# Kernel tuning notes

Hardware: AMD Instinct MI355X
Metric: run time of the kernel (lower is better)

## Reference

```python
import jax, jax.numpy as jnp
import numpy as np

# Dimensions: T total prefill tokens, S ragged segments (one adapter each),
# M target modules sharing this linear, r LoRA rank.
T, D_IN, D_OUT, R, M, S = 8192, 4096, 4096, 16, 2, 8


def setup_inputs() -> dict:
    key = jax.random.key(0)
    ks = jax.random.split(key, 6)
    x = jax.random.normal(ks[0], (T, D_IN), dtype=jnp.float32)
    W = jax.random.normal(ks[1], (D_OUT, D_IN), dtype=jnp.float32) * 0.02
    b = jax.random.normal(ks[2], (D_OUT,), dtype=jnp.float32) * 0.02
    # lora_A[m, s] = A.T of adapter s for target module m: [D_IN, R]
    lora_A = jax.random.normal(ks[3], (M, S, D_IN, R), dtype=jnp.float32) * 0.02
    # lora_B[m, s] = B.T: [R, D_OUT]
    lora_B = jax.random.normal(ks[4], (M, S, R, D_OUT), dtype=jnp.float32) * 0.02
    cu = jnp.sort(jax.random.randint(ks[5], (S + 1,), 0, T + 1, dtype=jnp.int32))
    cu = cu.at[0].set(0).at[-1].set(T)  # segment boundaries cover [0, T)
    return {"x": x, "W": W, "b": b, "lora_A": lora_A, "lora_B": lora_B,
            "cu_seqlen": cu}


def reference(x, W, b, lora_A, lora_B, cu_seqlen):
    # Base linear: out = x @ W.T + b
    out = x @ W.T + b
    tok = jnp.arange(x.shape[0])
    n_seg = lora_A.shape[1]
    # SGMV-style ragged LoRA: tokens in segment s use adapter s for every
    # target module m; contributions from all modules add into `out`.
    # Masking (instead of dynamic slicing) keeps shapes static / jit-friendly
    # and is exact: masked-out tokens contribute zero.
    for s in range(n_seg):
        mask = ((tok >= cu_seqlen[s]) & (tok < cu_seqlen[s + 1]))
        xm = x * mask.astype(x.dtype)[:, None]            # [T, D_IN], zero outside segment
        u = jnp.einsum('td,mdr->tmr', xm, lora_A[:, s])    # [T, M, R] low-rank down-proj
        out = out + jnp.einsum('tmr,mrD->tD', u, lora_B[:, s])  # up-proj, sum over modules
    return out
```

## Files before the change

kernel.cpp:

```cpp
#include <hip/hip_runtime.h>
#include <hip/hip_bf16.h>

#define T_TOK 8192
#define DIN   4096
#define DOUT  4096
#define RANK  16
#define NMOD  2
#define NSEG  8

typedef __attribute__((ext_vector_type(8))) short bf16x8;
typedef __attribute__((ext_vector_type(8))) unsigned short u16x8;
typedef __attribute__((ext_vector_type(4))) float f32x4;

__device__ inline unsigned short f2bf(float f) {
    union { float f; unsigned u; } v; v.f = f;
    unsigned r = v.u + 0x7FFFu + ((v.u >> 16) & 1u);
    return (unsigned short)(r >> 16);
}

__device__ inline void gload_lds16(const void* g, void* l) {
    __builtin_amdgcn_global_load_lds(
        (const __attribute__((address_space(1))) void*)g,
        (__attribute__((address_space(3))) void*)l, 16, 0, 0);
}

__global__ void cast2_bf16_kernel(const float* __restrict__ sa,
                                  unsigned short* __restrict__ da, int n8a,
                                  const float* __restrict__ sb,
                                  unsigned short* __restrict__ db, int n8b) {
    int i = blockIdx.x * blockDim.x + threadIdx.x;
    const float* s;
    unsigned short* d;
    size_t j;
    if (i < n8a) { s = sa; d = da; j = (size_t)i; }
    else if (i < n8a + n8b) { s = sb; d = db; j = (size_t)(i - n8a); }
    else return;
    const float4* s4 = (const float4*)s;
    float4 a = s4[2 * j];
    float4 b = s4[2 * j + 1];
    u16x8 o;
    o[0] = f2bf(a.x); o[1] = f2bf(a.y); o[2] = f2bf(a.z); o[3] = f2bf(a.w);
    o[4] = f2bf(b.x); o[5] = f2bf(b.y); o[6] = f2bf(b.z); o[7] = f2bf(b.w);
    *(u16x8*)(d + 8 * j) = o;
}

__global__ void prep_A_kernel(const float* __restrict__ A,
                              unsigned short* __restrict__ At) {
    int idx = blockIdx.x * 256 + threadIdx.x;
    int d   = idx & (DIN - 1);
    int smr = idx >> 12;
    int s   = smr >> 5, mr = smr & 31;
    int m   = mr >> 4,  r  = mr & 15;
    float v = A[(((size_t)(m * NSEG + s) * DIN) + d) * RANK + r];
    At[idx] = f2bf(v);
}

__global__ void prep_B_kernel(const float* __restrict__ B,
                              unsigned short* __restrict__ Bt) {
    int o  = blockIdx.x * 256 + threadIdx.x;
    int s  = o >> 12;
    int oc = o & (DOUT - 1);
    unsigned short tmp[32];
    for (int m = 0; m < NMOD; ++m)
        for (int r = 0; r < RANK; ++r)
            tmp[m * 16 + r] =
                f2bf(B[(((size_t)(m * NSEG + s) * RANK) + r) * DOUT + oc]);
    for (int k = 0; k < 4; ++k) {
        u16x8 v;
        for (int j = 0; j < 8; ++j) v[j] = tmp[k * 8 + j];
        *(u16x8*)(Bt + (size_t)o * 32 + k * 8) = v;
    }
}

__global__ __launch_bounds__(64) void u_gemm_kernel(
    const unsigned short* __restrict__ xb, const unsigned short* __restrict__ At,
    const int* __restrict__ cu, float* __restrict__ Pu) {
    int tile = blockIdx.x;
    int ky   = blockIdx.y;
    int lane = threadIdx.x;
    int l15  = lane & 15, lk = lane >> 4;
    int t0   = tile * 32;
    f32x4 acc[2][2] = {};
    bf16x8 zero = {};
    for (int s = 0; s < NSEG; ++s) {
        int lo = cu[s], hi = cu[s + 1];
        if (hi <= t0 || lo >= t0 + 32) continue;
        const unsigned short* atb = At + (size_t)(s * 32) * DIN;
        for (int kt = 0; kt < 32; ++kt) {
            int k0 = ky * 1024 + kt * 32 + lk * 8;
            bf16x8 a[2], b[2];
            for (int mi = 0; mi < 2; ++mi) {
                int row = t0 + mi * 16 + l15;
                bf16x8 av = *(const bf16x8*)(xb + (size_t)row * DIN + k0);
                a[mi] = (row >= lo && row < hi) ? av : zero;
            }
            for (int ni = 0; ni < 2; ++ni) {
                int mr = ni * 16 + l15;
                b[ni] = *(const bf16x8*)(atb + (size_t)mr * DIN + k0);
            }
            for (int mi = 0; mi < 2; ++mi)
                for (int ni = 0; ni < 2; ++ni)
                    acc[mi][ni] = __builtin_amdgcn_mfma_f32_16x16x32_bf16(
                        a[mi], b[ni], acc[mi][ni], 0, 0, 0);
        }
    }
    for (int mi = 0; mi < 2; ++mi)
        for (int ni = 0; ni < 2; ++ni)
            for (int j = 0; j < 4; ++j) {
                int t  = t0 + mi * 16 + lk * 4 + j;
                int mr = ni * 16 + l15;
                Pu[((size_t)ky * T_TOK + t) * 32 + mr] = acc[mi][ni][j];
            }
}

__global__ void reduce_u_kernel(const float* __restrict__ Pu,
                                unsigned short* __restrict__ ub) {
    int idx = blockIdx.x * 256 + threadIdx.x;
    const size_t STRIDE = (size_t)T_TOK * 32;
    float s = Pu[idx] + Pu[idx + STRIDE] + Pu[idx + 2 * STRIDE] + Pu[idx + 3 * STRIDE];
    ub[idx] = f2bf(s);
}


__device__ __forceinline__ bf16x8 frag(const char* mat, int row, int kbyte) {
    int rb = (row << 7) + kbyte;
    rb ^= ((rb >> 7) & 7) << 4;
    return *(const bf16x8*)(mat + rb);
}

#define STAGE_B(SB_, C_, K0_)                                                  \
  { int tb = tid * 16;                                                         \
    int lrow = (C_)*64 + (tb >> 7);                                            \
    int cb = (tb & 127) ^ ((lrow & 7) << 4);                                   \
    gload_lds16(wrow_g + (size_t)lrow * DIN + (K0_) + (cb >> 1),               \
                (SB_) + (C_)*8192 + tb); }

#define STAGE_A(SA_, C_, GB_, K0_)                                             \
  { int tb = tid * 16;                                                         \
    int lrow = (C_)*64 + (tb >> 7);                                            \
    int cb = (tb & 127) ^ ((lrow & 7) << 4);                                   \
    gload_lds16(xrow + (size_t)((GB_) + (tb >> 7)) * DIN + (K0_) + (cb >> 1),  \
                (SA_) + (C_)*8192 + tb); }

#define VMC(N_)                                                                \
    if ((N_) == 2)      asm volatile("s_waitcnt vmcnt(2)" ::: "memory");       \
    else if ((N_) == 0) asm volatile("s_waitcnt vmcnt(0)" ::: "memory");

#define PH_TAIL(VM_)                                                           \
    __builtin_amdgcn_s_barrier();                                              \
    asm volatile("s_waitcnt lgkmcnt(0)" ::: "memory");                         \
    __builtin_amdgcn_sched_barrier(0);                                         \
    __builtin_amdgcn_s_setprio(1);

#define PH_END(VM_)                                                            \
    __builtin_amdgcn_s_setprio(0);                                             \
    VMC(VM_);                                                                  \
    __builtin_amdgcn_s_barrier();

#define KSTEP(T_, CB_, STG_, VM0_, VM3_)                                       \
  {                                                                            \
    const char* cA  = lds + (CB_)*65536;                                       \
    const char* cBm = cA + 32768;                                              \
    char* sA = lds + (1 - (CB_))*65536;                                        \
    char* sB = sA + 32768;                                                     \
    const int k0n = ((T_) + 1) * 64;                                           \
    bf16x8 af[4], bf0[4], bf1[4];                                              \
    \
    for (int n = 0; n < 4; ++n) bf0[n] = frag(cBm, wcol + n*16 + l15, lk*16);  \
    for (int m = 0; m < 4; ++m) af[m]  = frag(cA, whalf*64 + m*16 + l15, lk*16);\
    if (STG_) { STAGE_B(sB, 0, k0n); STAGE_B(sB, 1, k0n); }                    \
    PH_TAIL(VM0_);                                                             \
    for (int m = 0; m < 4; ++m) for (int n = 0; n < 4; ++n)                    \
        acc[m][n] = __builtin_amdgcn_mfma_f32_16x16x32_bf16(                   \
            af[m], bf0[n], acc[m][n], 0, 0, 0);                                \
    PH_END(VM0_);                                                              \
           \
    for (int m = 0; m < 4; ++m)                                                \
        af[m] = frag(cA, 128 + whalf*64 + m*16 + l15, lk*16);                  \
    if (STG_) { STAGE_B(sB, 2, k0n); STAGE_B(sB, 3, k0n); }                    \
    PH_TAIL(-1);                                                               \
    for (int m = 0; m < 4; ++m) for (int n = 0; n < 4; ++n)                    \
        acc[4 + m][n] = __builtin_amdgcn_mfma_f32_16x16x32_bf16(               \
            af[m], bf0[n], acc[4 + m][n], 0, 0, 0);                            \
    PH_END(-1);                                                                \
    \
    for (int n = 0; n < 4; ++n)                                                \
        bf1[n] = frag(cBm, wcol + n*16 + l15, 64 + lk*16);                     \
    for (int m = 0; m < 4; ++m)                                                \
        af[m] = frag(cA, whalf*64 + m*16 + l15, 64 + lk*16);                   \
    if (STG_) { STAGE_A(sA, 0, 0, k0n); STAGE_A(sA, 1, 128, k0n); }            \
    PH_TAIL(-1);                                                               \
    for (int m = 0; m < 4; ++m) for (int n = 0; n < 4; ++n)                    \
        acc[m][n] = __builtin_amdgcn_mfma_f32_16x16x32_bf16(                   \
            af[m], bf1[n], acc[m][n], 0, 0, 0);                                \
    PH_END(-1);                                                                \
           \
    for (int m = 0; m < 4; ++m)                                                \
        af[m] = frag(cA, 128 + whalf*64 + m*16 + l15, 64 + lk*16);             \
    if (STG_) { STAGE_A(sA, 2, 64, k0n); STAGE_A(sA, 3, 192, k0n); }           \
    PH_TAIL(VM3_);                                                             \
    for (int m = 0; m < 4; ++m) for (int n = 0; n < 4; ++n)                    \
        acc[4 + m][n] = __builtin_amdgcn_mfma_f32_16x16x32_bf16(               \
            af[m], bf1[n], acc[4 + m][n], 0, 0, 0);                            \
    PH_END(VM3_);                                                              \
  }

__global__ __launch_bounds__(512, 2) void main_gemm_kernel(
    const unsigned short* __restrict__ xb, const unsigned short* __restrict__ wb,
    const unsigned short* __restrict__ ub, const unsigned short* __restrict__ bt,
    const float* __restrict__ bias, const int* __restrict__ cu,
    float* __restrict__ out) {
    __shared__ __attribute__((aligned(1024))) char lds[131072];
    int tid   = threadIdx.x;
    int w     = tid >> 6, lane = tid & 63;
    int l15   = lane & 15, lk = lane >> 4;
    int whalf = w >> 2;
    int wrow  = whalf * 128;
    int wcol  = (w & 3) * 64;
    int swz  = (blockIdx.x & 7) * 64 + (blockIdx.x >> 3);
    int row0 = (swz >> 4) * 256;
    int col0 = (swz & 15) * 256;

    const unsigned short* xrow   = xb + (size_t)row0 * DIN;
    const unsigned short* wrow_g = wb + (size_t)col0 * DIN;

    f32x4 acc[8][4] = {};

    {
        char* sA = lds;
        char* sB = lds + 32768;
        STAGE_B(sB, 0, 0); STAGE_B(sB, 1, 0);
        STAGE_B(sB, 2, 0); STAGE_B(sB, 3, 0);
        STAGE_A(sA, 0, 0, 0); STAGE_A(sA, 1, 128, 0);
        STAGE_A(sA, 2, 64, 0); STAGE_A(sA, 3, 192, 0);
    }
    asm volatile("s_waitcnt vmcnt(2)" ::: "memory");
    __builtin_amdgcn_s_barrier();

    #pragma unroll 1
    for (int t = 0; t < 62; t += 2) {
        KSTEP(t,     0, 1, 2, 2);
        KSTEP(t + 1, 1, 1, 2, 2);
    }
    KSTEP(62, 0, 1, 2, 2);
    KSTEP(63, 1, 0, 0, -1);

    bf16x8 zero = {};
    for (int s = 0; s < NSEG; ++s) {
        int lo = cu[s], hi = cu[s + 1];
        if (hi <= row0 || lo >= row0 + 256) continue;
        bf16x8 au[8], bu[4];
        for (int m = 0; m < 8; ++m) {
            int row = row0 + wrow + m * 16 + l15;
            bf16x8 v = *(const bf16x8*)(ub + (size_t)row * 32 + lk * 8);
            au[m] = (row >= lo && row < hi) ? v : zero;
        }
        for (int n = 0; n < 4; ++n) {
            int col = col0 + wcol + n * 16 + l15;
            bu[n] = *(const bf16x8*)(bt + ((size_t)s * DOUT + col) * 32 + lk * 8);
        }
        for (int m = 0; m < 8; ++m)
            for (int n = 0; n < 4; ++n)
                acc[m][n] = __builtin_amdgcn_mfma_f32_16x16x32_bf16(
                    au[m], bu[n], acc[m][n], 0, 0, 0);
    }

    float bv[4];
    for (int n = 0; n < 4; ++n) bv[n] = bias[col0 + wcol + n * 16 + l15];
    for (int m = 0; m < 8; ++m) {
        int rbase = row0 + wrow + m * 16 + lk * 4;
        for (int n = 0; n < 4; ++n) {
            int col = col0 + wcol + n * 16 + l15;
            for (int jj = 0; jj < 4; ++jj)
                out[(size_t)(rbase + jj) * DOUT + col] = acc[m][n][jj] + bv[n];
        }
    }
}

extern "C" void kernel_launch(void* const* d_in, const int* in_sizes, int n_in,
                              void* d_out, int out_size, void* d_ws, size_t ws_size,
                              hipStream_t stream) {
    const float* x  = (const float*)d_in[0];
    const float* W  = (const float*)d_in[1];
    const float* b  = (const float*)d_in[2];
    const float* lA = (const float*)d_in[3];
    const float* lB = (const float*)d_in[4];
    const int*   cu = (const int*)d_in[5];
    float* out = (float*)d_out;

    char* ws = (char*)d_ws;
    unsigned short* xb = (unsigned short*)(ws);
    unsigned short* wb = (unsigned short*)(ws + 67108864);
    unsigned short* At = (unsigned short*)(ws + 100663296);
    unsigned short* Bt = (unsigned short*)(ws + 102760448);
    float*          Pu = (float*)(ws + 104857600);
    unsigned short* ub = (unsigned short*)(ws + 109051904);

    const int n8x = T_TOK * DIN / 8, n8w = DOUT * DIN / 8;
    cast2_bf16_kernel<<<(n8x + n8w) / 256, 256, 0, stream>>>(x, xb, n8x, W, wb, n8w);
    prep_A_kernel<<<(NSEG * 32 * DIN) / 256, 256, 0, stream>>>(lA, At);
    prep_B_kernel<<<(NSEG * DOUT) / 256, 256, 0, stream>>>(lB, Bt);
    dim3 ug(T_TOK / 32, 4);
    u_gemm_kernel<<<ug, 64, 0, stream>>>(xb, At, cu, Pu);
    reduce_u_kernel<<<(T_TOK * 32) / 256, 256, 0, stream>>>(Pu, ub);
    dim3 mg(32 * 16);
    main_gemm_kernel<<<mg, 512, 0, stream>>>(xb, wb, ub, Bt, b, cu, out);
}
```

Baseline: 316.0 us.

## Software-pipeline LDS fragment loads across k-steps with ping-pong registers

Reworks the inner GEMM k-step so that the A and B fragments for the next step are read from LDS during the last MFMA phase of the current step. This uses ping-pong fragment registers (afP/afQ, bf0/bf1) that persist across steps, so each MFMA block overlaps the fragment reads for the following block. Global-to-LDS staging is redistributed across the phases (B chunks interleaved with A chunks), with explicit vmcnt waits and barriers placed between phases. The aim is to hide LDS read latency and smooth memory issue. The cost is higher register pressure under 2 blocks/CU and more fragile wait-count correctness.

```diff
diff --git a/kernel.cpp b/kernel.cpp
--- a/kernel.cpp
+++ b/kernel.cpp
@@ -142,67 +142,61 @@
     gload_lds16(xrow + (size_t)((GB_) + (tb >> 7)) * DIN + (K0_) + (cb >> 1),  \
                 (SA_) + (C_)*8192 + tb); }
 
-#define VMC(N_)                                                                \
-    if ((N_) == 2)      asm volatile("s_waitcnt vmcnt(2)" ::: "memory");       \
-    else if ((N_) == 0) asm volatile("s_waitcnt vmcnt(0)" ::: "memory");
-
-#define PH_TAIL(VM_)                                                           \
-    __builtin_amdgcn_s_barrier();                                              \
-    asm volatile("s_waitcnt lgkmcnt(0)" ::: "memory");                         \
-    __builtin_amdgcn_sched_barrier(0);                                         \
-    __builtin_amdgcn_s_setprio(1);
-
-#define PH_END(VM_)                                                            \
-    __builtin_amdgcn_s_setprio(0);                                             \
-    VMC(VM_);                                                                  \
-    __builtin_amdgcn_s_barrier();
-
-#define KSTEP(T_, CB_, STG_, VM0_, VM3_)                                       \
+#define MFMA16(ACCBASE_, AF_, BF_)                                             \
+    __builtin_amdgcn_s_setprio(1);                                             \
+    for (int m = 0; m < 4; ++m)                                                \
+        for (int n = 0; n < 4; ++n)                                            \
+            acc[(ACCBASE_) + m][n] = __builtin_amdgcn_mfma_f32_16x16x32_bf16(  \
+                AF_[m], BF_[n], acc[(ACCBASE_) + m][n], 0, 0, 0);              \
+    __builtin_amdgcn_s_setprio(0);
+
+#define KSTEP(T_, CB_, STG_, LAST_)                                            \
   {                                                                            \
-    const char* cA  = lds + (CB_)*65536;                                       \
-    const char* cBm = cA + 32768;                                              \
+    const char* cA = lds + (CB_)*65536;                                        \
+    const char* cB = cA + 32768;                                               \
     char* sA = lds + (1 - (CB_))*65536;                                        \
     char* sB = sA + 32768;                                                     \
     const int k0n = ((T_) + 1) * 64;                                           \
-    bf16x8 af[4], bf0[4], bf1[4];                                              \
     \
-    for (int n = 0; n < 4; ++n) bf0[n] = frag(cBm, wcol + n*16 + l15, lk*16);  \
-    for (int m = 0; m < 4; ++m) af[m]  = frag(cA, whalf*64 + m*16 + l15, lk*16);\
-    if (STG_) { STAGE_B(sB, 0, k0n); STAGE_B(sB, 1, k0n); }                    \
-    PH_TAIL(VM0_);                                                             \
-    for (int m = 0; m < 4; ++m) for (int n = 0; n < 4; ++n)                    \
-        acc[m][n] = __builtin_amdgcn_mfma_f32_16x16x32_bf16(                   \
-            af[m], bf0[n], acc[m][n], 0, 0, 0);                                \
-    PH_END(VM0_);                                                              \
-           \
+    if (STG_) {                                                                \
+        STAGE_B(sB, 0, k0n); STAGE_B(sB, 1, k0n); STAGE_A(sA, 0, 0, k0n);      \
+        asm volatile("s_waitcnt vmcnt(3)" ::: "memory");                       \
+    } else {                                                                   \
+        asm volatile("s_waitcnt vmcnt(0)" ::: "memory");                       \
+    }                                                                          \
+    __builtin_amdgcn_s_barrier();                                              \
     for (int m = 0; m < 4; ++m)                                                \
-        af[m] = frag(cA, 128 + whalf*64 + m*16 + l15, lk*16);                  \
-    if (STG_) { STAGE_B(sB, 2, k0n); STAGE_B(sB, 3, k0n); }                    \
-    PH_TAIL(-1);                                                               \
-    for (int m = 0; m < 4; ++m) for (int n = 0; n < 4; ++n)                    \
-        acc[4 + m][n] = __builtin_amdgcn_mfma_f32_16x16x32_bf16(               \
-            af[m], bf0[n], acc[4 + m][n], 0, 0, 0);                            \
-    PH_END(-1);                                                                \
+        afQ[m] = frag(cA, 128 + whalf*64 + m*16 + l15, lk*16);                 \
+    MFMA16(0, afP, bf0);                                                       \
+    __builtin_amdgcn_s_barrier();                                              \
     \
+    if (STG_) { STAGE_B(sB, 2, k0n); STAGE_B(sB, 3, k0n);                      \
+                STAGE_A(sA, 1, 128, k0n); }                                    \
+    __builtin_amdgcn_s_barrier();                                              \
     for (int n = 0; n < 4; ++n)                                                \
-        bf1[n] = frag(cBm, wcol + n*16 + l15, 64 + lk*16);                     \
+        bf1[n] = frag(cB, wcol + n*16 + l15, 64 + lk*16);                      \
     for (int m = 0; m < 4; ++m)                                                \
-        af[m] = frag(cA, whalf*64 + m*16 + l15, 64 + lk*16);                   \
-    if (STG_) { STAGE_A(sA, 0, 0, k0n); STAGE_A(sA, 1, 128, k0n); }            \
-    PH_TAIL(-1);                                                               \
-    for (int m = 0; m < 4; ++m) for (int n = 0; n < 4; ++n)                    \
-        acc[m][n] = __builtin_amdgcn_mfma_f32_16x16x32_bf16(                   \
-            af[m], bf1[n], acc[m][n], 0, 0, 0);                                \
-    PH_END(-1);                                                                \
-           \
+        afP[m] = frag(cA, whalf*64 + m*16 + l15, 64 + lk*16);                  \
+    MFMA16(4, afQ, bf0);                                                       \
+    __builtin_amdgcn_s_barrier();                                              \
+               \
+    if (STG_) { STAGE_A(sA, 2, 64, k0n); STAGE_A(sA, 3, 192, k0n); }           \
+    __builtin_amdgcn_s_barrier();                                              \
     for (int m = 0; m < 4; ++m)                                                \
-        af[m] = frag(cA, 128 + whalf*64 + m*16 + l15, 64 + lk*16);             \
-    if (STG_) { STAGE_A(sA, 2, 64, k0n); STAGE_A(sA, 3, 192, k0n); }           \
-    PH_TAIL(VM3_);                                                             \
-    for (int m = 0; m < 4; ++m) for (int n = 0; n < 4; ++n)                    \
-        acc[4 + m][n] = __builtin_amdgcn_mfma_f32_16x16x32_bf16(               \
-            af[m], bf1[n], acc[4 + m][n], 0, 0, 0);                            \
-    PH_END(VM3_);                                                              \
+        afQ[m] = frag(cA, 128 + whalf*64 + m*16 + l15, 64 + lk*16);            \
+    MFMA16(0, afP, bf1);                                                       \
+    __builtin_amdgcn_s_barrier();                                              \
+    \
+    asm volatile("s_waitcnt vmcnt(2)" ::: "memory");                           \
+    __builtin_amdgcn_s_barrier();                                              \
+    if (!(LAST_)) {                                                            \
+        for (int n = 0; n < 4; ++n)                                            \
+            bf0[n] = frag(sB, wcol + n*16 + l15, lk*16);                       \
+        for (int m = 0; m < 4; ++m)                                            \
+            afP[m] = frag(sA, whalf*64 + m*16 + l15, lk*16);                   \
+    }                                                                          \
+    MFMA16(4, afQ, bf1);                                                       \
+    __builtin_amdgcn_s_barrier();                                              \
   }
 
 __global__ __launch_bounds__(512, 2) void main_gemm_kernel(
@@ -225,25 +219,29 @@
     const unsigned short* wrow_g = wb + (size_t)col0 * DIN;
 
     f32x4 acc[8][4] = {};
+    bf16x8 bf0[4], bf1[4], afP[4], afQ[4];
 
     {
         char* sA = lds;
         char* sB = lds + 32768;
-        STAGE_B(sB, 0, 0); STAGE_B(sB, 1, 0);
-        STAGE_B(sB, 2, 0); STAGE_B(sB, 3, 0);
-        STAGE_A(sA, 0, 0, 0); STAGE_A(sA, 1, 128, 0);
+        STAGE_B(sB, 0, 0); STAGE_B(sB, 1, 0); STAGE_A(sA, 0, 0, 0);
+        STAGE_B(sB, 2, 0); STAGE_B(sB, 3, 0); STAGE_A(sA, 1, 128, 0);
         STAGE_A(sA, 2, 64, 0); STAGE_A(sA, 3, 192, 0);
     }
     asm volatile("s_waitcnt vmcnt(2)" ::: "memory");
     __builtin_amdgcn_s_barrier();
+    for (int n = 0; n < 4; ++n)
+        bf0[n] = frag(lds + 32768, wcol + n*16 + l15, lk*16);
+    for (int m = 0; m < 4; ++m)
+        afP[m] = frag(lds, whalf*64 + m*16 + l15, lk*16);
 
     #pragma unroll 1
     for (int t = 0; t < 62; t += 2) {
-        KSTEP(t,     0, 1, 2, 2);
-        KSTEP(t + 1, 1, 1, 2, 2);
-    }
-    KSTEP(62, 0, 1, 2, 2);
-    KSTEP(63, 1, 0, 0, -1);
+        KSTEP(t,     0, 1, 0);
+        KSTEP(t + 1, 1, 1, 0);
+    }
+    KSTEP(62, 0, 1, 0);
+    KSTEP(63, 1, 0, 1);
 
     bf16x8 zero = {};
     for (int s = 0; s < NSEG; ++s) {
```

Measured after the change: 327.5 us. +3.7%, slower.
